# Kernel optimization log

Hardware: AMD Instinct MI355X
Metric: run time of the kernel (lower is better)

## Reference

```python
import jax, jax.numpy as jnp
import numpy as np

EPS = 1e-8

def setup_inputs() -> dict:
    key = jax.random.key(0)
    k1, k2 = jax.random.split(key)
    B, T = 512, 65536
    preds = jax.random.normal(k1, (B, T), dtype=jnp.float32)
    labels = jax.random.normal(k2, (B, T), dtype=jnp.float32)
    return {"preds": preds, "labels": labels}

def reference(preds, labels):
    # Batched per-sample statistics over all non-batch dims (here last axis).
    mean_x = jnp.mean(preds, axis=1)                      # [B]
    mean_y = jnp.mean(labels, axis=1)                     # [B]
    xc = preds - mean_x[:, None]
    yc = labels - mean_y[:, None]
    var_x = jnp.mean(xc * xc, axis=1)
    var_y = jnp.mean(yc * yc, axis=1)
    cov_xy = jnp.mean(xc * yc, axis=1)
    ccc = 2.0 * cov_xy / (var_x + var_y + (mean_x - mean_y) ** 2 + EPS)
    return jnp.mean(1.0 - ccc)
```

## Files before the change

### kernel.cpp

```cpp
#include <hip/hip_runtime.h>

#define CCC_EPS 1e-8
#define SEGS 4
#define TPB 256
#define PER_THREAD 16

typedef float floatx4 __attribute__((ext_vector_type(4)));

__global__ __launch_bounds__(TPB, 4) void ccc_partial_kernel(
    const float* __restrict__ preds,
    const float* __restrict__ labels,
    float* __restrict__ partial,
    int T)
{
    const int seg = blockIdx.x & (SEGS - 1);
    const int row = blockIdx.x >> 2;
    const int seg4 = (T >> 2) / SEGS;
    const size_t base4 = (size_t)row * (size_t)(T >> 2) + (size_t)seg * seg4;
    const floatx4* __restrict__ p4 = (const floatx4*)preds + base4;
    const floatx4* __restrict__ l4 = (const floatx4*)labels + base4;

    float sx = 0.f, sy = 0.f, sxx = 0.f, syy = 0.f, sxy = 0.f;

    #pragma unroll 8
    for (int k = 0; k < PER_THREAD; ++k) {
        const int i = threadIdx.x + k * TPB;
        floatx4 x = p4[i];
        floatx4 y = l4[i];
        sx  += x.x + x.y + x.z + x.w;
        sy  += y.x + y.y + y.z + y.w;
        sxx = fmaf(x.x, x.x, sxx); sxx = fmaf(x.y, x.y, sxx);
        sxx = fmaf(x.z, x.z, sxx); sxx = fmaf(x.w, x.w, sxx);
        syy = fmaf(y.x, y.x, syy); syy = fmaf(y.y, y.y, syy);
        syy = fmaf(y.z, y.z, syy); syy = fmaf(y.w, y.w, syy);
        sxy = fmaf(x.x, y.x, sxy); sxy = fmaf(x.y, y.y, sxy);
        sxy = fmaf(x.z, y.z, sxy); sxy = fmaf(x.w, y.w, sxy);
    }

    #pragma unroll
    for (int off = 32; off > 0; off >>= 1) {
        sx  += __shfl_down(sx,  off);
        sy  += __shfl_down(sy,  off);
        sxx += __shfl_down(sxx, off);
        syy += __shfl_down(syy, off);
        sxy += __shfl_down(sxy, off);
    }

    __shared__ float red[4][5];
    const int wave = threadIdx.x >> 6;
    const int lane = threadIdx.x & 63;
    if (lane == 0) {
        red[wave][0] = sx;  red[wave][1] = sy;  red[wave][2] = sxx;
        red[wave][3] = syy; red[wave][4] = sxy;
    }
    __syncthreads();

    if (threadIdx.x == 0) {
        float t0 = red[0][0] + red[1][0] + red[2][0] + red[3][0];
        float t1 = red[0][1] + red[1][1] + red[2][1] + red[3][1];
        float t2 = red[0][2] + red[1][2] + red[2][2] + red[3][2];
        float t3 = red[0][3] + red[1][3] + red[2][3] + red[3][3];
        float t4 = red[0][4] + red[1][4] + red[2][4] + red[3][4];
        float* dst = partial + ((size_t)row * SEGS + seg) * 5;
        dst[0] = t0; dst[1] = t1; dst[2] = t2; dst[3] = t3; dst[4] = t4;
    }
}

__global__ __launch_bounds__(512) void ccc_final_kernel(
    const float* __restrict__ partial,
    float* __restrict__ out,
    int B, int T)
{
    float loss_sum = 0.f;
    for (int b = threadIdx.x; b < B; b += 512) {
        double tsx = 0, tsy = 0, tsxx = 0, tsyy = 0, tsxy = 0;
        const float* src = partial + (size_t)b * SEGS * 5;
        #pragma unroll
        for (int s = 0; s < SEGS; ++s) {
            tsx  += src[s * 5 + 0];
            tsy  += src[s * 5 + 1];
            tsxx += src[s * 5 + 2];
            tsyy += src[s * 5 + 3];
            tsxy += src[s * 5 + 4];
        }
        const double inv = 1.0 / (double)T;
        const double mx = tsx * inv;
        const double my = tsy * inv;
        const double vx = tsxx * inv - mx * mx;
        const double vy = tsyy * inv - my * my;
        const double cov = tsxy * inv - mx * my;
        const double d = mx - my;
        const double ccc = 2.0 * cov / (vx + vy + d * d + CCC_EPS);
        loss_sum += (float)(1.0 - ccc);
    }

    #pragma unroll
    for (int off = 32; off > 0; off >>= 1) loss_sum += __shfl_down(loss_sum, off);

    __shared__ float red[8];
    const int wave = threadIdx.x >> 6;
    const int lane = threadIdx.x & 63;
    if (lane == 0) red[wave] = loss_sum;
    __syncthreads();
    if (threadIdx.x == 0) {
        float t = 0.f;
        #pragma unroll
        for (int w = 0; w < 8; ++w) t += red[w];
        out[0] = t / (float)B;
    }
}

extern "C" void kernel_launch(void* const* d_in, const int* in_sizes, int n_in,
                              void* d_out, int out_size, void* d_ws, size_t ws_size,
                              hipStream_t stream) {
    const float* preds  = (const float*)d_in[0];
    const float* labels = (const float*)d_in[1];
    float* out = (float*)d_out;

    const int T = 65536;
    const int B = in_sizes[0] / T;

    float* partial = (float*)d_ws;

    ccc_partial_kernel<<<B * SEGS, TPB, 0, stream>>>(preds, labels, partial, T);
    ccc_final_kernel<<<1, 512, 0, stream>>>(partial, out, B, T);
}
```

Measured before the change: 278.6 us.

## Stream inputs through LDS with async global_load_lds software pipeline

Replaces the direct register loads with `global_load_lds` transfers into a per-wave 8-slot LDS ring buffer. Loads are issued 6 steps ahead and explicit `s_waitcnt vmcnt` waits gate each consume step. The goal is to keep more memory requests in flight and to decouple load issue from the reduction arithmetic. The cost is 64 KB of LDS per block, which limits how many blocks fit per CU. It also adds an extra LDS round-trip and relies on hand-computed wait counts for correctness.

```diff
diff --git a/kernel.cpp b/kernel.cpp
--- a/kernel.cpp
+++ b/kernel.cpp
@@ -1,11 +1,26 @@
 #include <hip/hip_runtime.h>
+#include <stdint.h>
 
 #define CCC_EPS 1e-8
 #define SEGS 4
 #define TPB 256
 #define PER_THREAD 16
+#define DEPTH 8
+#define AHEAD 6
 
 typedef float floatx4 __attribute__((ext_vector_type(4)));
+
+template <int N>
+__device__ __forceinline__ void wait_vmcnt() {
+    asm volatile("s_waitcnt vmcnt(%0)" :: "n"(N) : "memory");
+}
+
+__device__ __forceinline__ void gld_lds16(const void* g, void* l) {
+    __builtin_amdgcn_global_load_lds(
+        (const __attribute__((address_space(1))) uint32_t*)(uintptr_t)g,
+        (__attribute__((address_space(3))) uint32_t*)(uint32_t)(uintptr_t)l,
+        16, 0, 2 );
+}
 
 __global__ __launch_bounds__(TPB, 4) void ccc_partial_kernel(
     const float* __restrict__ preds,
@@ -20,22 +35,56 @@
     const floatx4* __restrict__ p4 = (const floatx4*)preds + base4;
     const floatx4* __restrict__ l4 = (const floatx4*)labels + base4;
 
+    __shared__ floatx4 lx[4][DEPTH][64];
+    __shared__ floatx4 ly[4][DEPTH][64];
+
+    const int wave = threadIdx.x >> 6;
+    const int lane = threadIdx.x & 63;
+
     float sx = 0.f, sy = 0.f, sxx = 0.f, syy = 0.f, sxy = 0.f;
 
-    #pragma unroll 8
-    for (int k = 0; k < PER_THREAD; ++k) {
-        const int i = threadIdx.x + k * TPB;
-        floatx4 x = p4[i];
-        floatx4 y = l4[i];
-        sx  += x.x + x.y + x.z + x.w;
-        sy  += y.x + y.y + y.z + y.w;
-        sxx = fmaf(x.x, x.x, sxx); sxx = fmaf(x.y, x.y, sxx);
-        sxx = fmaf(x.z, x.z, sxx); sxx = fmaf(x.w, x.w, sxx);
-        syy = fmaf(y.x, y.x, syy); syy = fmaf(y.y, y.y, syy);
-        syy = fmaf(y.z, y.z, syy); syy = fmaf(y.w, y.w, syy);
-        sxy = fmaf(x.x, y.x, sxy); sxy = fmaf(x.y, y.y, sxy);
-        sxy = fmaf(x.z, y.z, sxy); sxy = fmaf(x.w, y.w, sxy);
-    }
+#define ISSUE(s)                                                              \
+    do {                                                                      \
+        if ((s) < PER_THREAD) {                                               \
+            const int _sl = (s) & (DEPTH - 1);                                \
+            gld_lds16(&p4[(size_t)(s) * TPB + threadIdx.x], &lx[wave][_sl][0]); \
+            gld_lds16(&l4[(size_t)(s) * TPB + threadIdx.x], &ly[wave][_sl][0]); \
+        }                                                                     \
+    } while (0)
+
+#define CONSUME(k)                                                            \
+    do {                                                                      \
+        const int _sl = (k) & (DEPTH - 1);                                    \
+        floatx4 x = lx[wave][_sl][lane];                                      \
+        floatx4 y = ly[wave][_sl][lane];                                      \
+        sx  += x.x + x.y + x.z + x.w;                                         \
+        sy  += y.x + y.y + y.z + y.w;                                         \
+        sxx = fmaf(x.x, x.x, sxx); sxx = fmaf(x.y, x.y, sxx);                 \
+        sxx = fmaf(x.z, x.z, sxx); sxx = fmaf(x.w, x.w, sxx);                 \
+        syy = fmaf(y.x, y.x, syy); syy = fmaf(y.y, y.y, syy);                 \
+        syy = fmaf(y.z, y.z, syy); syy = fmaf(y.w, y.w, syy);                 \
+        sxy = fmaf(x.x, y.x, sxy); sxy = fmaf(x.y, y.y, sxy);                 \
+        sxy = fmaf(x.z, y.z, sxy); sxy = fmaf(x.w, y.w, sxy);                 \
+    } while (0)
+
+#define VMN(k) (((k) + AHEAD < PER_THREAD) ? (2 * AHEAD) : (2 * (PER_THREAD - 1 - (k))))
+#define STEP(k)                                                               \
+    do {                                                                      \
+        ISSUE((k) + AHEAD);                                                   \
+        wait_vmcnt<VMN(k)>();                                                 \
+        CONSUME(k);                                                           \
+    } while (0)
+
+    ISSUE(0); ISSUE(1); ISSUE(2); ISSUE(3); ISSUE(4); ISSUE(5);
+    STEP(0);  STEP(1);  STEP(2);  STEP(3);
+    STEP(4);  STEP(5);  STEP(6);  STEP(7);
+    STEP(8);  STEP(9);  STEP(10); STEP(11);
+    STEP(12); STEP(13); STEP(14); STEP(15);
+
+#undef STEP
+#undef VMN
+#undef CONSUME
+#undef ISSUE
 
     #pragma unroll
     for (int off = 32; off > 0; off >>= 1) {
@@ -47,8 +96,6 @@
     }
 
     __shared__ float red[4][5];
-    const int wave = threadIdx.x >> 6;
-    const int lane = threadIdx.x & 63;
     if (lane == 0) {
         red[wave][0] = sx;  red[wave][1] = sy;  red[wave][2] = sxx;
         red[wave][3] = syy; red[wave][4] = sxy;
```

Result: faster. 247.0 us (median of 2 runs) (-11.4%).
